# Kernel tuning notes

Hardware: AMD Instinct MI355X
Metric: run time of the kernel (lower is better)

The kernel has to match this reference:

```python
import jax, jax.numpy as jnp
import numpy as np

B, S, H, DH = 8, 1024, 16, 64
D = H * DH  # d_model = 1024
M_ALPHA = -1e9


def setup_inputs() -> dict:
    key = jax.random.key(0)
    ks = jax.random.split(key, 11)
    scale = 1.0 / np.sqrt(D)
    x = jax.random.normal(ks[0], (B, S, D), dtype=jnp.float32)
    # 0/1 padding mask, shape [B, S, 1] (1 = masked position)
    mask = (jax.random.uniform(ks[1], (B, S, 1)) < 0.25).astype(jnp.float32)
    mk = lambda k: jax.random.normal(k, (D, D), dtype=jnp.float32) * scale
    return {
        "x": x,
        "mask": mask,
        "wq_w": mk(ks[2]), "wq_b": jnp.zeros((D,), jnp.float32),
        "wk_w": mk(ks[3]), "wk_b": jnp.zeros((D,), jnp.float32),
        "wv_w": mk(ks[4]), "wv_b": jnp.zeros((D,), jnp.float32),
        "wo_w": mk(ks[5]), "wo_b": jnp.zeros((D,), jnp.float32),
    }


def _split_heads(t):
    # [B, S, D] -> [B, H, S, DH]
    return t.reshape(B, S, H, DH).transpose(0, 2, 1, 3)


def reference(x, mask, wq_w, wq_b, wk_w, wk_b, wv_w, wv_b, wo_w, wo_b):
    q = _split_heads(x @ wq_w + wq_b)  # [B,H,S,DH]
    k = _split_heads(x @ wk_w + wk_b)
    v = _split_heads(x @ wv_w + wv_b)

    logits = jnp.einsum("bhqd,bhkd->bhqk", q, k) / jnp.sqrt(
        jnp.asarray(DH, jnp.float32))
    qk_values = logits  # pre-mask scaled logits (temperature == 0.0 -> no-op)

    # QK mask path: mask [B,S,1] -> tile to [B,S,S] rows (m[b,i,j] = mask[b,i]),
    # then symmetrize (square) -> mask[b,i] + mask[b,j], clamp at 1.
    m = mask[:, :, 0]                               # [B,S]
    mask_qk = jnp.minimum(1.0, m[:, :, None] + m[:, None, :])  # [B,S,S]
    logits = logits + mask_qk[:, None, :, :] * M_ALPHA

    attn = jax.nn.softmax(logits, axis=-1)          # [B,H,S,S]
    z = jnp.einsum("bhqk,bhkd->bhqd", attn, v)      # [B,H,S,DH]
    z = z.transpose(0, 2, 1, 3).reshape(B, S, D)
    out = z @ wo_w + wo_b
    return (out, attn, qk_values, q, k, v)
```

## Files before the change

### kernel.cpp

```cpp
#include <hip/hip_runtime.h>
#include <hip/hip_bf16.h>
#include <stdint.h>

#define BB 8
#define SS 1024
#define HH 16
#define DHD 64
#define DD 1024

typedef __attribute__((ext_vector_type(8))) short bf16x8;
typedef __attribute__((ext_vector_type(4))) float f32x4;

__device__ __forceinline__ unsigned short f2bf(float f) {
  unsigned u = __builtin_bit_cast(unsigned, f);
  u += 0x7fffu + ((u >> 16) & 1u);
  return (unsigned short)(u >> 16);
}

__device__ __forceinline__ unsigned swz(unsigned a) { return a ^ ((a >> 3) & 0x70u); }

#define GLOAD16(gp, lp)                                                        \
  __builtin_amdgcn_global_load_lds(                                            \
      (const __attribute__((address_space(1))) unsigned int*)(gp),             \
      (__attribute__((address_space(3))) unsigned int*)(lp), 16, 0, 0)

#define MFMA16(a, b, c) __builtin_amdgcn_mfma_f32_16x16x32_bf16(a, b, c, 0, 0, 0)

__global__ __launch_bounds__(256) void cvt_x_kernel(const float* __restrict__ x,
                                                    unsigned short* __restrict__ xb) {
  int i = blockIdx.x * 256 + threadIdx.x;
  float4 v = ((const float4*)x)[i];
  ushort4 o;
  o.x = f2bf(v.x); o.y = f2bf(v.y); o.z = f2bf(v.z); o.w = f2bf(v.w);
  ((ushort4*)xb)[i] = o;
}

__global__ __launch_bounds__(256) void transpose_w_kernel(
    const float* __restrict__ w0, const float* __restrict__ w1,
    const float* __restrict__ w2, const float* __restrict__ w3,
    unsigned short* __restrict__ o0, unsigned short* __restrict__ o1,
    unsigned short* __restrict__ o2, unsigned short* __restrict__ o3) {
  __shared__ float tile[32][33];
  const float* src; unsigned short* dst;
  if (blockIdx.z == 0)      { src = w0; dst = o0; }
  else if (blockIdx.z == 1) { src = w1; dst = o1; }
  else if (blockIdx.z == 2) { src = w2; dst = o2; }
  else                      { src = w3; dst = o3; }
  int n0 = blockIdx.x * 32, k0 = blockIdx.y * 32;
  int tx = threadIdx.x, ty = threadIdx.y;
#pragma unroll
  for (int j = 0; j < 32; j += 8)
    tile[ty + j][tx] = src[(size_t)(k0 + ty + j) * DD + n0 + tx];
  __syncthreads();
#pragma unroll
  for (int j = 0; j < 32; j += 8)
    dst[(size_t)(n0 + ty + j) * DD + k0 + tx] = f2bf(tile[tx][ty + j]);
}

__global__ __launch_bounds__(256) void proj_gemm_kernel(
    const unsigned short* __restrict__ xb,
    const unsigned short* __restrict__ wqt, const unsigned short* __restrict__ wkt,
    const unsigned short* __restrict__ wvt,
    const float* __restrict__ bq, const float* __restrict__ bk, const float* __restrict__ bv,
    float* __restrict__ qo, float* __restrict__ ko, float* __restrict__ vo,
    unsigned short* __restrict__ qb, unsigned short* __restrict__ kbf,
    unsigned short* __restrict__ vt) {
  __shared__ __align__(128) unsigned short As[128 * 64];
  __shared__ __align__(128) unsigned short Bs[128 * 64];
  const int tid = threadIdx.x, lane = tid & 63, w = tid >> 6;
  const int wr = (w >> 1) * 64, wc = (w & 1) * 64;
  const int m0 = blockIdx.x * 128;
  const int mat = blockIdx.y >> 3;
  const int n0 = (blockIdx.y & 7) * 128;
  const unsigned short* Bg = (mat == 0) ? wqt : (mat == 1) ? wkt : wvt;
  const float* bias = (mat == 0) ? bq : (mat == 1) ? bk : bv;

  f32x4 acc[4][4];
  f32x4 z4 = {0.f, 0.f, 0.f, 0.f};
#pragma unroll
  for (int i = 0; i < 4; ++i)
#pragma unroll
    for (int j = 0; j < 4; ++j) acc[i][j] = z4;

  for (int kt = 0; kt < 1024; kt += 64) {
    __syncthreads();
#pragma unroll
    for (int i = 0; i < 4; ++i) {
      unsigned obase = (unsigned)(w * 4096 + i * 1024);
      unsigned a = swz(obase + (unsigned)lane * 16);
      GLOAD16((const char*)xb + ((size_t)(m0 + (int)(a >> 7)) * 1024 + kt) * 2 + (a & 127),
              (char*)As + obase);
      GLOAD16((const char*)Bg + ((size_t)(n0 + (int)(a >> 7)) * 1024 + kt) * 2 + (a & 127),
              (char*)Bs + obase);
    }
    __syncthreads();
#pragma unroll
    for (int ks = 0; ks < 2; ++ks) {
      bf16x8 af[4], bfr[4];
#pragma unroll
      for (int mi = 0; mi < 4; ++mi) {
        unsigned a = (unsigned)((wr + mi * 16 + (lane & 15)) * 128 + ks * 64 + ((lane >> 4) * 16));
        af[mi] = *(const bf16x8*)((const char*)As + swz(a));
      }
#pragma unroll
      for (int ni = 0; ni < 4; ++ni) {
        unsigned a = (unsigned)((wc + ni * 16 + (lane & 15)) * 128 + ks * 64 + ((lane >> 4) * 16));
        bfr[ni] = *(const bf16x8*)((const char*)Bs + swz(a));
      }
#pragma unroll
      for (int mi = 0; mi < 4; ++mi)
#pragma unroll
        for (int ni = 0; ni < 4; ++ni)
          acc[mi][ni] = MFMA16(af[mi], bfr[ni], acc[mi][ni]);
    }
  }

  float* fo = (mat == 0) ? qo : (mat == 1) ? ko : vo;
#pragma unroll
  for (int mi = 0; mi < 4; ++mi)
#pragma unroll
    for (int ni = 0; ni < 4; ++ni) {
      int col = n0 + wc + ni * 16 + (lane & 15);
      float bs = bias[col];
#pragma unroll
      for (int r = 0; r < 4; ++r) {
        int row = m0 + wr + mi * 16 + ((lane >> 4) << 2) + r;
        float v = acc[mi][ni][r] + bs;
        int b = row >> 10, s = row & 1023, h = col >> 6, dh = col & 63;
        size_t bh = (size_t)(b * HH + h);
        fo[(bh * SS + s) * DHD + dh] = v;
        if (mat == 2) vt[(bh * DHD + dh) * SS + s] = f2bf(v);
        else ((mat == 0) ? qb : kbf)[(bh * SS + s) * DHD + dh] = f2bf(v);
      }
    }
}

__global__ __launch_bounds__(256) void attn_kernel(
    const unsigned short* __restrict__ qb, const unsigned short* __restrict__ kb,
    const unsigned short* __restrict__ vt, const float* __restrict__ mask,
    float* __restrict__ qk_out, float* __restrict__ attn_out,
    unsigned short* __restrict__ zb) {
  __shared__ __align__(128) unsigned short kbuf[64 * 64];
  __shared__ __align__(128) unsigned short vbuf[64 * 64];
  __shared__ __align__(128) unsigned short pbuf[4][16 * 64];
  __shared__ __align__(16) float mbuf[SS];

  const int tid = threadIdx.x, lane = tid & 63, w = tid >> 6;
  const int qt = blockIdx.x, h = blockIdx.y, b = blockIdx.z;
  const int bh = b * HH + h;
  const int r0 = qt * 64 + w * 16;

  ((float4*)mbuf)[tid] = ((const float4*)(mask + (size_t)b * SS))[tid];

  bf16x8 aq[2];
  {
    const unsigned short* p = qb + (size_t)bh * SS * DHD + (size_t)(r0 + (lane & 15)) * DHD + ((lane >> 4) * 8);
    aq[0] = *(const bf16x8*)p;
    aq[1] = *(const bf16x8*)(p + 32);
  }
  float mq[4];
#pragma unroll
  for (int r = 0; r < 4; ++r)
    mq[r] = mask[(size_t)b * SS + r0 + ((lane >> 4) << 2) + r];

  const unsigned short* kbase = kb + (size_t)bh * SS * DHD;
  const char* vbase = (const char*)(vt + (size_t)bh * DHD * SS);
  float* qkb = qk_out + (size_t)bh * SS * SS;
  float* atb = attn_out + (size_t)bh * SS * SS;

  float m_run[4], l_run[4];
#pragma unroll
  for (int r = 0; r < 4; ++r) { m_run[r] = -INFINITY; l_run[r] = 0.f; }

  for (int kt = 0; kt < 16; ++kt) {
    int k0 = kt * 64;
    __syncthreads();
#pragma unroll
    for (int i = 0; i < 2; ++i) {
      unsigned obase = (unsigned)(w * 2048 + i * 1024);
      unsigned a = swz(obase + (unsigned)lane * 16);
      GLOAD16((const char*)(kbase + (size_t)k0 * 64) + a, (char*)kbuf + obase);
    }
    __syncthreads();
    float sm[4][4];
#pragma unroll
    for (int ct = 0; ct < 4; ++ct) {
      f32x4 acc = {0.f, 0.f, 0.f, 0.f};
#pragma unroll
      for (int ks = 0; ks < 2; ++ks) {
        unsigned a = (unsigned)((ct * 16 + (lane & 15)) * 128 + ks * 64 + ((lane >> 4) * 16));
        bf16x8 bk = *(const bf16x8*)((const char*)kbuf + swz(a));
        acc = MFMA16(aq[ks], bk, acc);
      }
      int col = k0 + ct * 16 + (lane & 15);
      float mk = mbuf[col];
      float* qrow = qkb + (size_t)(r0 + ((lane >> 4) << 2)) * SS + col;
#pragma unroll
      for (int r = 0; r < 4; ++r) {
        float logit = acc[r] * 0.125f;
        qrow[(size_t)r * SS] = logit;
        float t = fminf(mq[r] + mk, 1.f);
        sm[ct][r] = logit + t * (-1.0e9f);
      }
    }
#pragma unroll
    for (int r = 0; r < 4; ++r) {
      float mx = fmaxf(fmaxf(sm[0][r], sm[1][r]), fmaxf(sm[2][r], sm[3][r]));
#pragma unroll
      for (int d = 1; d < 16; d <<= 1) mx = fmaxf(mx, __shfl_xor(mx, d, 64));
      float m_new = fmaxf(m_run[r], mx);
      float es = __expf(sm[0][r] - m_new) + __expf(sm[1][r] - m_new) +
                 __expf(sm[2][r] - m_new) + __expf(sm[3][r] - m_new);
#pragma unroll
      for (int d = 1; d < 16; d <<= 1) es += __shfl_xor(es, d, 64);
      l_run[r] = l_run[r] * __expf(m_run[r] - m_new) + es;
      m_run[r] = m_new;
    }
  }

  float inv_l[4];
#pragma unroll
  for (int r = 0; r < 4; ++r) inv_l[r] = 1.0f / l_run[r];

  f32x4 zacc[4];
#pragma unroll
  for (int dt = 0; dt < 4; ++dt) zacc[dt] = (f32x4){0.f, 0.f, 0.f, 0.f};

  for (int kt = 0; kt < 16; ++kt) {
    int k0 = kt * 64;
    __syncthreads();
#pragma unroll
    for (int i = 0; i < 2; ++i) {
      unsigned obase = (unsigned)(w * 2048 + i * 1024);
      unsigned a = swz(obase + (unsigned)lane * 16);
      GLOAD16((const char*)(kbase + (size_t)k0 * 64) + a, (char*)kbuf + obase);
      GLOAD16(vbase + (size_t)(a >> 7) * (SS * 2) + (size_t)k0 * 2 + (a & 127),
              (char*)vbuf + obase);
    }
    __syncthreads();
#pragma unroll
    for (int ct = 0; ct < 4; ++ct) {
      f32x4 acc = {0.f, 0.f, 0.f, 0.f};
#pragma unroll
      for (int ks = 0; ks < 2; ++ks) {
        unsigned a = (unsigned)((ct * 16 + (lane & 15)) * 128 + ks * 64 + ((lane >> 4) * 16));
        bf16x8 bk = *(const bf16x8*)((const char*)kbuf + swz(a));
        acc = MFMA16(aq[ks], bk, acc);
      }
      int col = k0 + ct * 16 + (lane & 15);
      float mk = mbuf[col];
#pragma unroll
      for (int r = 0; r < 4; ++r) {
        float logit = acc[r] * 0.125f;
        float t = fminf(mq[r] + mk, 1.f);
        float e = __expf(logit + t * (-1.0e9f) - m_run[r]);
        float pn = e * inv_l[r];
        atb[(size_t)(r0 + ((lane >> 4) << 2) + r) * SS + col] = pn;
        unsigned a2 = (unsigned)((((lane >> 4) << 2) + r) * 128 + (ct * 16 + (lane & 15)) * 2);
        *(unsigned short*)((char*)pbuf[w] + swz(a2)) = f2bf(pn);
      }
    }
#pragma unroll
    for (int dt = 0; dt < 4; ++dt) {
#pragma unroll
      for (int ks = 0; ks < 2; ++ks) {
        unsigned ap = (unsigned)((lane & 15) * 128 + ks * 64 + ((lane >> 4) * 16));
        bf16x8 pa = *(const bf16x8*)((const char*)pbuf[w] + swz(ap));
        unsigned av = (unsigned)((dt * 16 + (lane & 15)) * 128 + ks * 64 + ((lane >> 4) * 16));
        bf16x8 bv = *(const bf16x8*)((const char*)vbuf + swz(av));
        zacc[dt] = MFMA16(pa, bv, zacc[dt]);
      }
    }
  }

#pragma unroll
  for (int dt = 0; dt < 4; ++dt)
#pragma unroll
    for (int r = 0; r < 4; ++r) {
      int srow = r0 + ((lane >> 4) << 2) + r;
      int dcol = dt * 16 + (lane & 15);
      zb[((size_t)b * SS + srow) * DD + h * 64 + dcol] = f2bf(zacc[dt][r]);
    }
}

__global__ __launch_bounds__(256) void out_gemm_kernel(
    const unsigned short* __restrict__ zb, const unsigned short* __restrict__ wot,
    const float* __restrict__ bo, float* __restrict__ outp) {
  __shared__ __align__(128) unsigned short As[128 * 64];
  __shared__ __align__(128) unsigned short Bs[128 * 64];
  const int tid = threadIdx.x, lane = tid & 63, w = tid >> 6;
  const int wr = (w >> 1) * 64, wc = (w & 1) * 64;
  const int m0 = blockIdx.x * 128;
  const int n0 = blockIdx.y * 128;

  f32x4 acc[4][4];
  f32x4 z4 = {0.f, 0.f, 0.f, 0.f};
#pragma unroll
  for (int i = 0; i < 4; ++i)
#pragma unroll
    for (int j = 0; j < 4; ++j) acc[i][j] = z4;

  for (int kt = 0; kt < 1024; kt += 64) {
    __syncthreads();
#pragma unroll
    for (int i = 0; i < 4; ++i) {
      unsigned obase = (unsigned)(w * 4096 + i * 1024);
      unsigned a = swz(obase + (unsigned)lane * 16);
      GLOAD16((const char*)zb + ((size_t)(m0 + (int)(a >> 7)) * 1024 + kt) * 2 + (a & 127),
              (char*)As + obase);
      GLOAD16((const char*)wot + ((size_t)(n0 + (int)(a >> 7)) * 1024 + kt) * 2 + (a & 127),
              (char*)Bs + obase);
    }
    __syncthreads();
#pragma unroll
    for (int ks = 0; ks < 2; ++ks) {
      bf16x8 af[4], bfr[4];
#pragma unroll
      for (int mi = 0; mi < 4; ++mi) {
        unsigned a = (unsigned)((wr + mi * 16 + (lane & 15)) * 128 + ks * 64 + ((lane >> 4) * 16));
        af[mi] = *(const bf16x8*)((const char*)As + swz(a));
      }
#pragma unroll
      for (int ni = 0; ni < 4; ++ni) {
        unsigned a = (unsigned)((wc + ni * 16 + (lane & 15)) * 128 + ks * 64 + ((lane >> 4) * 16));
        bfr[ni] = *(const bf16x8*)((const char*)Bs + swz(a));
      }
#pragma unroll
      for (int mi = 0; mi < 4; ++mi)
#pragma unroll
        for (int ni = 0; ni < 4; ++ni)
          acc[mi][ni] = MFMA16(af[mi], bfr[ni], acc[mi][ni]);
    }
  }
#pragma unroll
  for (int mi = 0; mi < 4; ++mi)
#pragma unroll
    for (int ni = 0; ni < 4; ++ni) {
      int col = n0 + wc + ni * 16 + (lane & 15);
      float bs = bo[col];
#pragma unroll
      for (int r = 0; r < 4; ++r) {
        int row = m0 + wr + mi * 16 + ((lane >> 4) << 2) + r;
        outp[(size_t)row * DD + col] = acc[mi][ni][r] + bs;
      }
    }
}

extern "C" void kernel_launch(void* const* d_in, const int* in_sizes, int n_in,
                              void* d_out, int out_size, void* d_ws, size_t ws_size,
                              hipStream_t stream) {
  const float* x    = (const float*)d_in[0];
  const float* mask = (const float*)d_in[1];
  const float* wq_w = (const float*)d_in[2];
  const float* wq_b = (const float*)d_in[3];
  const float* wk_w = (const float*)d_in[4];
  const float* wk_b = (const float*)d_in[5];
  const float* wv_w = (const float*)d_in[6];
  const float* wv_b = (const float*)d_in[7];
  const float* wo_w = (const float*)d_in[8];
  const float* wo_b = (const float*)d_in[9];

  float* outp = (float*)d_out;
  float* attn = outp + (size_t)8388608;
  float* qk   = attn + (size_t)134217728;
  float* qo   = qk + (size_t)134217728;
  float* ko   = qo + (size_t)8388608;
  float* vo   = ko + (size_t)8388608;

  char* ws = (char*)d_ws;
  unsigned short* xb  = (unsigned short*)(ws + 0);
  unsigned short* wqt = (unsigned short*)(ws + 16777216);
  unsigned short* wkt = (unsigned short*)(ws + 18874368);
  unsigned short* wvt = (unsigned short*)(ws + 20971520);
  unsigned short* wot = (unsigned short*)(ws + 23068672);
  unsigned short* qb  = (unsigned short*)(ws + 25165824);
  unsigned short* kb  = (unsigned short*)(ws + 41943040);
  unsigned short* vt  = (unsigned short*)(ws + 58720256);
  unsigned short* zb  = (unsigned short*)(ws + 75497472);

  cvt_x_kernel<<<8192, 256, 0, stream>>>(x, xb);
  transpose_w_kernel<<<dim3(32, 32, 4), dim3(32, 8), 0, stream>>>(
      wq_w, wk_w, wv_w, wo_w, wqt, wkt, wvt, wot);
  proj_gemm_kernel<<<dim3(64, 24), 256, 0, stream>>>(
      xb, wqt, wkt, wvt, wq_b, wk_b, wv_b, qo, ko, vo, qb, kb, vt);
  attn_kernel<<<dim3(16, 16, 8), 256, 0, stream>>>(qb, kb, vt, mask, qk, attn, zb);
  out_gemm_kernel<<<dim3(64, 8), 256, 0, stream>>>(zb, wot, wo_b, outp);
}
```

Baseline: 517.2 us.

## Stage V transpose through LDS, fold softmax scale into Q, use nontemporal stores

The V projection epilogue now transposes its tile through shared memory and writes the transposed bf16 V with 16-byte coalesced stores, replacing scattered 2-byte writes. The 1/sqrt(dh) scale is folded into the bf16 Q copy, which removes a multiply per logit in the attention kernel. Large fp32 output writes (q/k/v, qk logits, attn, out) use nontemporal stores to limit cache pollution. The attention grid is flattened so that consecutive blocks cover different heads and batches of the same query tile. Folding the scale before the bf16 rounding changes rounding slightly.

```diff
diff --git a/kernel.cpp b/kernel.cpp
--- a/kernel.cpp
+++ b/kernel.cpp
@@ -65,8 +65,9 @@
     float* __restrict__ qo, float* __restrict__ ko, float* __restrict__ vo,
     unsigned short* __restrict__ qb, unsigned short* __restrict__ kbf,
     unsigned short* __restrict__ vt) {
-  __shared__ __align__(128) unsigned short As[128 * 64];
-  __shared__ __align__(128) unsigned short Bs[128 * 64];
+  __shared__ __align__(128) unsigned short smem[2 * 128 * 64];
+  unsigned short* As = smem;
+  unsigned short* Bs = smem + 128 * 64;
   const int tid = threadIdx.x, lane = tid & 63, w = tid >> 6;
   const int wr = (w >> 1) * 64, wc = (w & 1) * 64;
   const int m0 = blockIdx.x * 128;
@@ -116,6 +117,9 @@
   }
 
   float* fo = (mat == 0) ? qo : (mat == 1) ? ko : vo;
+  __syncthreads();
+  unsigned short* T = smem;
+
 #pragma unroll
   for (int mi = 0; mi < 4; ++mi)
 #pragma unroll
@@ -128,11 +132,35 @@
         float v = acc[mi][ni][r] + bs;
         int b = row >> 10, s = row & 1023, h = col >> 6, dh = col & 63;
         size_t bh = (size_t)(b * HH + h);
-        fo[(bh * SS + s) * DHD + dh] = v;
-        if (mat == 2) vt[(bh * DHD + dh) * SS + s] = f2bf(v);
-        else ((mat == 0) ? qb : kbf)[(bh * SS + s) * DHD + dh] = f2bf(v);
-      }
-    }
+        __builtin_nontemporal_store(v, &fo[(bh * SS + s) * DHD + dh]);
+        if (mat == 2) {
+          int sl = wr + mi * 16 + ((lane >> 4) << 2) + r;
+          int dl = wc + ni * 16 + (lane & 15);
+          T[dl * 128 + (sl ^ ((dl & 7) << 4))] = f2bf(v);
+        } else if (mat == 0) {
+          qb[(bh * SS + s) * DHD + dh] = f2bf(v * 0.125f);
+        } else {
+          kbf[(bh * SS + s) * DHD + dh] = f2bf(v);
+        }
+      }
+    }
+
+  if (mat == 2) {
+    __syncthreads();
+    int row = tid >> 1;
+    int half = tid & 1;
+    int colg = n0 + row;
+    int h2 = colg >> 6, dh2 = colg & 63;
+    int b = m0 >> 10;
+    int sg0 = (m0 & 1023) + half * 64;
+    unsigned short* dst = vt + (((size_t)(b * HH + h2)) * DHD + dh2) * SS + sg0;
+#pragma unroll
+    for (int j = 0; j < 8; ++j) {
+      int sc = half * 64 + j * 8;
+      bf16x8 vv = *(const bf16x8*)&T[row * 128 + (sc ^ ((row & 7) << 4))];
+      *(bf16x8*)(dst + j * 8) = vv;
+    }
+  }
 }
 
 __global__ __launch_bounds__(256) void attn_kernel(
@@ -146,8 +174,9 @@
   __shared__ __align__(16) float mbuf[SS];
 
   const int tid = threadIdx.x, lane = tid & 63, w = tid >> 6;
-  const int qt = blockIdx.x, h = blockIdx.y, b = blockIdx.z;
-  const int bh = b * HH + h;
+  const int fid = blockIdx.x;
+  const int bh = fid & 127, qt = fid >> 7;
+  const int b = bh >> 4, h = bh & 15;
   const int r0 = qt * 64 + w * 16;
 
   ((float4*)mbuf)[tid] = ((const float4*)(mask + (size_t)b * SS))[tid];
@@ -197,8 +226,8 @@
       float* qrow = qkb + (size_t)(r0 + ((lane >> 4) << 2)) * SS + col;
 #pragma unroll
       for (int r = 0; r < 4; ++r) {
-        float logit = acc[r] * 0.125f;
-        qrow[(size_t)r * SS] = logit;
+        float logit = acc[r];
+        __builtin_nontemporal_store(logit, &qrow[(size_t)r * SS]);
         float t = fminf(mq[r] + mk, 1.f);
         sm[ct][r] = logit + t * (-1.0e9f);
       }
@@ -251,11 +280,11 @@
       float mk = mbuf[col];
 #pragma unroll
       for (int r = 0; r < 4; ++r) {
-        float logit = acc[r] * 0.125f;
+        float logit = acc[r];
         float t = fminf(mq[r] + mk, 1.f);
         float e = __expf(logit + t * (-1.0e9f) - m_run[r]);
         float pn = e * inv_l[r];
-        atb[(size_t)(r0 + ((lane >> 4) << 2) + r) * SS + col] = pn;
+        __builtin_nontemporal_store(pn, &atb[(size_t)(r0 + ((lane >> 4) << 2) + r) * SS + col]);
         unsigned a2 = (unsigned)((((lane >> 4) << 2) + r) * 128 + (ct * 16 + (lane & 15)) * 2);
         *(unsigned short*)((char*)pbuf[w] + swz(a2)) = f2bf(pn);
       }
@@ -341,7 +370,7 @@
 #pragma unroll
       for (int r = 0; r < 4; ++r) {
         int row = m0 + wr + mi * 16 + ((lane >> 4) << 2) + r;
-        outp[(size_t)row * DD + col] = acc[mi][ni][r] + bs;
+        __builtin_nontemporal_store(acc[mi][ni][r] + bs, &outp[(size_t)row * DD + col]);
       }
     }
 }
@@ -383,6 +412,6 @@
       wq_w, wk_w, wv_w, wo_w, wqt, wkt, wvt, wot);
   proj_gemm_kernel<<<dim3(64, 24), 256, 0, stream>>>(
       xb, wqt, wkt, wvt, wq_b, wk_b, wv_b, qo, ko, vo, qb, kb, vt);
-  attn_kernel<<<dim3(16, 16, 8), 256, 0, stream>>>(qb, kb, vt, mask, qk, attn, zb);
+  attn_kernel<<<2048, 256, 0, stream>>>(qb, kb, vt, mask, qk, attn, zb);
   out_gemm_kernel<<<dim3(64, 8), 256, 0, stream>>>(zb, wot, wo_b, outp);
 }
```

Measured after the change: 522.3 us. Within noise of the previous version (+1.0%).
